# Optimization experiments

Hardware: AMD Instinct MI355X
Metric: run time of the kernel (lower is better)

Reference implementation:

```python
import jax, jax.numpy as jnp
import numpy as np

B, IN_CAPS, IN_DIM = 64, 512, 128
NUM_CAPS, DIM_CAPS, NUM_ROUTING = 32, 32, 3


def squash(x, axis=-1):
    sn = jnp.sum(x * x, axis=axis, keepdims=True)
    return (sn / (1.0 + sn)) * x / (jnp.sqrt(sn) + 1e-8)


def setup_inputs() -> dict:
    key = jax.random.key(0)
    k1, k2, k3 = jax.random.split(key, 3)
    input_tensor = jax.random.normal(k1, (B, IN_CAPS, IN_DIM), dtype=jnp.float32)
    W = 0.001 * jax.random.normal(k2, (NUM_CAPS, IN_DIM, DIM_CAPS), dtype=jnp.float32)
    b0 = jax.random.uniform(k3, (B, NUM_CAPS, IN_CAPS, 1), dtype=jnp.float32)
    return {"input_tensor": input_tensor, "W": W, "b0": b0}


def reference(input_tensor, W, b0):
    # u_hat: (B, num_caps, in_caps, dim_caps)
    u_hat = jnp.einsum('bid,ndc->bnic', input_tensor, W)
    temp_u_hat = jax.lax.stop_gradient(u_hat)
    b = b0
    for _ in range(NUM_ROUTING - 1):
        c = jax.nn.softmax(b, axis=1)            # (B, num_caps, in_caps, 1)
        s = jnp.sum(c * temp_u_hat, axis=2)      # (B, num_caps, dim_caps)
        v = squash(s)
        uv = jnp.einsum('bnic,bnc->bni', temp_u_hat, v)[..., None]
        b = b + uv
    c = jax.nn.softmax(b, axis=1)
    s = jnp.sum(c * u_hat, axis=2)
    return squash(s)                             # (B, num_caps, dim_caps)
```

## Files before the change

### kernel.cpp

```cpp
#include <hip/hip_runtime.h>
#include <math.h>

#define Bsz 64
#define IC  512
#define KD  128
#define NC  32
#define DC  32
#define CHUNK 64
#define NCH   8
#define NBLK  512
#define NTHR  256
#define NTHRB 128

#define CSTR 36
#define BSTR 68
#define WSTR 33

#define CXP_SZ (Bsz * NCH * NC * KD)
#define WV_SZ  (Bsz * NC * KD)

__device__ __forceinline__ int xaddr(int i, int kq) {
    return i * KD + ((((kq) + (i >> 2)) & 31) << 2);
}

__global__ __launch_bounds__(NTHR)
void kACX(const float* __restrict__ bb_in, const float* __restrict__ x_g,
          const float* __restrict__ wv_g, float* __restrict__ bb_out,
          float* __restrict__ cxp, int do_uv, int write_bb)
{
    __shared__ float x_s[CHUNK * KD];
    __shared__ float bb_s[NC * BSTR];
    __shared__ float scr[KD * CSTR];

    const int t = threadIdx.x, blk = blockIdx.x;
    const int b = blk >> 3, ch = blk & 7, i0g = ch * CHUNK;

    for (int rep = 0; rep < 8; ++rep) {
        int v = t + rep * NTHR;
        int i = v >> 5, kq = v & 31;
        *(float4*)(x_s + xaddr(i, kq)) =
            *(const float4*)(x_g + ((size_t)(b * IC + i0g + i)) * KD + (kq << 2));
    }
    for (int rep = 0; rep < 2; ++rep) {
        int v = t + rep * NTHR;
        int n = v >> 4, i4 = v & 15;
        *(float4*)(bb_s + n * BSTR + (i4 << 2)) =
            *(const float4*)(bb_in + ((size_t)(b * NC + n)) * IC + i0g + (i4 << 2));
    }
    if (do_uv) {
        for (int rep = 0; rep < 4; ++rep) {
            const int n = t & 31;
            const int k4 = (t >> 5) + (rep << 3);
            float4 v4 = *(const float4*)(wv_g + ((size_t)(b * NC) + n) * KD + (k4 << 2));
            scr[(k4 * 4 + 0) * CSTR + n] = v4.x;
            scr[(k4 * 4 + 1) * CSTR + n] = v4.y;
            scr[(k4 * 4 + 2) * CSTR + n] = v4.z;
            scr[(k4 * 4 + 3) * CSTR + n] = v4.w;
        }
    }
    __syncthreads();

    if (do_uv) {
        if (t < 128) {
            const int tn = t & 7, ti = t >> 3;
            const int n0 = tn << 2, i0 = ti << 2;
            float4 a0 = {0,0,0,0}, a1 = {0,0,0,0}, a2 = {0,0,0,0}, a3 = {0,0,0,0};
            for (int kq = 0; kq < 32; ++kq) {
                const float4 xr0 = *(const float4*)(x_s + xaddr(i0 + 0, kq));
                const float4 xr1 = *(const float4*)(x_s + xaddr(i0 + 1, kq));
                const float4 xr2 = *(const float4*)(x_s + xaddr(i0 + 2, kq));
                const float4 xr3 = *(const float4*)(x_s + xaddr(i0 + 3, kq));
                const float4 w0 = *(const float4*)(scr + (kq * 4 + 0) * CSTR + n0);
                const float4 w1 = *(const float4*)(scr + (kq * 4 + 1) * CSTR + n0);
                const float4 w2 = *(const float4*)(scr + (kq * 4 + 2) * CSTR + n0);
                const float4 w3 = *(const float4*)(scr + (kq * 4 + 3) * CSTR + n0);
                a0.x += xr0.x*w0.x + xr0.y*w1.x + xr0.z*w2.x + xr0.w*w3.x;
                a0.y += xr0.x*w0.y + xr0.y*w1.y + xr0.z*w2.y + xr0.w*w3.y;
                a0.z += xr0.x*w0.z + xr0.y*w1.z + xr0.z*w2.z + xr0.w*w3.z;
                a0.w += xr0.x*w0.w + xr0.y*w1.w + xr0.z*w2.w + xr0.w*w3.w;
                a1.x += xr1.x*w0.x + xr1.y*w1.x + xr1.z*w2.x + xr1.w*w3.x;
                a1.y += xr1.x*w0.y + xr1.y*w1.y + xr1.z*w2.y + xr1.w*w3.y;
                a1.z += xr1.x*w0.z + xr1.y*w1.z + xr1.z*w2.z + xr1.w*w3.z;
                a1.w += xr1.x*w0.w + xr1.y*w1.w + xr1.z*w2.w + xr1.w*w3.w;
                a2.x += xr2.x*w0.x + xr2.y*w1.x + xr2.z*w2.x + xr2.w*w3.x;
                a2.y += xr2.x*w0.y + xr2.y*w1.y + xr2.z*w2.y + xr2.w*w3.y;
                a2.z += xr2.x*w0.z + xr2.y*w1.z + xr2.z*w2.z + xr2.w*w3.z;
                a2.w += xr2.x*w0.w + xr2.y*w1.w + xr2.z*w2.w + xr2.w*w3.w;
                a3.x += xr3.x*w0.x + xr3.y*w1.x + xr3.z*w2.x + xr3.w*w3.x;
                a3.y += xr3.x*w0.y + xr3.y*w1.y + xr3.z*w2.y + xr3.w*w3.y;
                a3.z += xr3.x*w0.z + xr3.y*w1.z + xr3.z*w2.z + xr3.w*w3.z;
                a3.w += xr3.x*w0.w + xr3.y*w1.w + xr3.z*w2.w + xr3.w*w3.w;
            }
            bb_s[(n0+0)*BSTR + i0+0] += a0.x; bb_s[(n0+1)*BSTR + i0+0] += a0.y;
            bb_s[(n0+2)*BSTR + i0+0] += a0.z; bb_s[(n0+3)*BSTR + i0+0] += a0.w;
            bb_s[(n0+0)*BSTR + i0+1] += a1.x; bb_s[(n0+1)*BSTR + i0+1] += a1.y;
            bb_s[(n0+2)*BSTR + i0+1] += a1.z; bb_s[(n0+3)*BSTR + i0+1] += a1.w;
            bb_s[(n0+0)*BSTR + i0+2] += a2.x; bb_s[(n0+1)*BSTR + i0+2] += a2.y;
            bb_s[(n0+2)*BSTR + i0+2] += a2.z; bb_s[(n0+3)*BSTR + i0+2] += a2.w;
            bb_s[(n0+0)*BSTR + i0+3] += a3.x; bb_s[(n0+1)*BSTR + i0+3] += a3.y;
            bb_s[(n0+2)*BSTR + i0+3] += a3.z; bb_s[(n0+3)*BSTR + i0+3] += a3.w;
        }
        __syncthreads();
        if (write_bb) {
            for (int rep = 0; rep < 2; ++rep) {
                int v = t + rep * NTHR;
                int n = v >> 4, i4 = v & 15;
                *(float4*)(bb_out + ((size_t)(b * NC + n)) * IC + i0g + (i4 << 2)) =
                    *(const float4*)(bb_s + n * BSTR + (i4 << 2));
            }
        }
    }

    if (t < CHUNK) {
        const int ii = t;
        float m = -1e30f;
        #pragma unroll
        for (int n = 0; n < NC; ++n) m = fmaxf(m, bb_s[n * BSTR + ii]);
        float e[NC]; float sum = 0.f;
        #pragma unroll
        for (int n = 0; n < NC; ++n) { float ev = __expf(bb_s[n * BSTR + ii] - m); e[n] = ev; sum += ev; }
        const float inv = 1.f / sum;
        float* crow = scr + ii * CSTR;
        #pragma unroll
        for (int n = 0; n < NC; ++n) crow[n] = e[n] * inv;
    }
    __syncthreads();

    const int tn = t & 7, tk = t >> 3;
    const int n0 = tn << 2;
    float4 acc0 = {0,0,0,0}, acc1 = {0,0,0,0}, acc2 = {0,0,0,0}, acc3 = {0,0,0,0};
    for (int ii = 0; ii < CHUNK; ++ii) {
        const float4 c4 = *(const float4*)(scr + ii * CSTR + n0);
        const float4 x4 = *(const float4*)(x_s + xaddr(ii, tk));
        acc0.x += c4.x*x4.x; acc0.y += c4.x*x4.y; acc0.z += c4.x*x4.z; acc0.w += c4.x*x4.w;
        acc1.x += c4.y*x4.x; acc1.y += c4.y*x4.y; acc1.z += c4.y*x4.z; acc1.w += c4.y*x4.w;
        acc2.x += c4.z*x4.x; acc2.y += c4.z*x4.y; acc2.z += c4.z*x4.z; acc2.w += c4.z*x4.w;
        acc3.x += c4.w*x4.x; acc3.y += c4.w*x4.y; acc3.z += c4.w*x4.z; acc3.w += c4.w*x4.w;
    }
    float* base = cxp + ((size_t)(b * NCH + ch)) * NC * KD + (tk << 2);
    *(float4*)(base + (size_t)(n0 + 0) * KD) = acc0;
    *(float4*)(base + (size_t)(n0 + 1) * KD) = acc1;
    *(float4*)(base + (size_t)(n0 + 2) * KD) = acc2;
    *(float4*)(base + (size_t)(n0 + 3) * KD) = acc3;
}

__global__ __launch_bounds__(NTHRB)
void kB(const float* __restrict__ cxp, const float* __restrict__ W_g,
        float* __restrict__ wv_g, float* __restrict__ out_g, int final_)
{
    __shared__ float w_s[KD * WSTR];
    __shared__ float cxs[4 * KD];
    __shared__ float vs_s[4][DC];

    const int t = threadIdx.x, blk = blockIdx.x;
    const int pb_n = blk & 31, pb_b0 = (blk >> 5) * 4;

    for (int rep = 0; rep < 8; ++rep) {
        int v = t + rep * NTHRB;
        int k = v >> 3, d0 = (v & 7) << 2;
        float4 w4 = *(const float4*)(W_g + (size_t)pb_n * KD * DC + (v << 2));
        float* dst = w_s + k * WSTR + d0;
        dst[0] = w4.x; dst[1] = w4.y; dst[2] = w4.z; dst[3] = w4.w;
    }
    {
        const int bsub = t >> 5, k4 = t & 31;
        float4 s4 = {0,0,0,0};
        const float* p = cxp + (((size_t)(pb_b0 + bsub) * NCH) * NC + pb_n) * KD + (k4 << 2);
        #pragma unroll
        for (int c2 = 0; c2 < NCH; ++c2) {
            float4 v4 = *(const float4*)(p + (size_t)c2 * NC * KD);
            s4.x += v4.x; s4.y += v4.y; s4.z += v4.z; s4.w += v4.w;
        }
        *(float4*)(cxs + bsub * KD + (k4 << 2)) = s4;
    }
    __syncthreads();

    const int bsub = t >> 5, d = t & 31;
    float s = 0.f;
    const float* crow = cxs + bsub * KD;
    for (int k = 0; k < KD; ++k) s += crow[k] * w_s[k * WSTR + d];
    float sn = s * s;
    #pragma unroll
    for (int off = 1; off < 32; off <<= 1) sn += __shfl_xor(sn, off, 64);
    const float vv = s * (sn / ((1.f + sn) * (sqrtf(sn) + 1e-8f)));

    if (final_) {
        out_g[((size_t)(pb_b0 + bsub) * NC + pb_n) * DC + d] = vv;
    } else {
        vs_s[bsub][d] = vv;
        __syncthreads();
        const int k = t;
        float a0 = 0.f, a1 = 0.f, a2 = 0.f, a3 = 0.f;
        #pragma unroll
        for (int dd = 0; dd < DC; ++dd) {
            const float wk = w_s[k * WSTR + dd];
            a0 += wk * vs_s[0][dd];
            a1 += wk * vs_s[1][dd];
            a2 += wk * vs_s[2][dd];
            a3 += wk * vs_s[3][dd];
        }
        size_t base = (((size_t)pb_b0 * NC) + pb_n) * KD + k;
        wv_g[base                      ] = a0;
        wv_g[base + 1 * (size_t)NC * KD] = a1;
        wv_g[base + 2 * (size_t)NC * KD] = a2;
        wv_g[base + 3 * (size_t)NC * KD] = a3;
    }
}

extern "C" void kernel_launch(void* const* d_in, const int* in_sizes, int n_in,
                              void* d_out, int out_size, void* d_ws, size_t ws_size,
                              hipStream_t stream) {
    const float* x  = (const float*)d_in[0];
    const float* W  = (const float*)d_in[1];
    const float* b0 = (const float*)d_in[2];
    float* out = (float*)d_out;

    float* cxp   = (float*)d_ws;
    float* wv    = cxp + CXP_SZ;
    float* bb_ws = wv + WV_SZ;

    kACX<<<NBLK, NTHR, 0, stream>>>(b0, x, nullptr, nullptr, cxp, 0, 0);
    kB  <<<NBLK, NTHRB, 0, stream>>>(cxp, W, wv, out, 0);
    kACX<<<NBLK, NTHR, 0, stream>>>(b0, x, wv, bb_ws, cxp, 1, 1);
    kB  <<<NBLK, NTHRB, 0, stream>>>(cxp, W, wv, out, 0);
    kACX<<<NBLK, NTHR, 0, stream>>>(bb_ws, x, wv, nullptr, cxp, 1, 0);
    kB  <<<NBLK, NTHRB, 0, stream>>>(cxp, W, wv, out, 1);
}
```

Measured before the change: 126.9 us.

## Fuse six routing kernels into one persistent kernel with grid barriers

Replaces the three alternating pairs of kACX/kB launches with a single persistent kernel of 256 blocks. The blocks synchronise through atomic-counter grid barriers, which are reset by a memset before the launch. Each block handles two input-capsule chunks per phase and eight batches in the reduce/squash phase. The aim is to remove launch gaps and tail effects between the six launches. In exchange it relies on all 256 blocks being co-resident, halves the block count, and adds spin-wait costs plus a memset launch.

Result: slower. 277.0 us (+118.4%).

```diff
diff --git a/kernel.cpp b/kernel.cpp
--- a/kernel.cpp
+++ b/kernel.cpp
@@ -8,9 +8,8 @@
 #define DC  32
 #define CHUNK 64
 #define NCH   8
-#define NBLK  512
+#define GBLK  256
 #define NTHR  256
-#define NTHRB 128
 
 #define CSTR 36
 #define BSTR 68
@@ -18,192 +17,217 @@
 
 #define CXP_SZ (Bsz * NCH * NC * KD)
 #define WV_SZ  (Bsz * NC * KD)
+#define BB_SZ  (Bsz * NC * IC)
 
 __device__ __forceinline__ int xaddr(int i, int kq) {
     return i * KD + ((((kq) + (i >> 2)) & 31) << 2);
 }
 
-__global__ __launch_bounds__(NTHR)
-void kACX(const float* __restrict__ bb_in, const float* __restrict__ x_g,
-          const float* __restrict__ wv_g, float* __restrict__ bb_out,
-          float* __restrict__ cxp, int do_uv, int write_bb)
+__device__ __forceinline__ void gridbar(unsigned* ctr, int slot) {
+    __syncthreads();
+    if (threadIdx.x == 0) {
+        __threadfence();
+        unsigned* c = ctr + slot;
+        __hip_atomic_fetch_add(c, 1u, __ATOMIC_ACQ_REL, __HIP_MEMORY_SCOPE_AGENT);
+        unsigned tries = 0;
+        while (__hip_atomic_load(c, __ATOMIC_ACQUIRE, __HIP_MEMORY_SCOPE_AGENT) < GBLK &&
+               tries < (1u << 20)) {
+            ++tries;
+            __builtin_amdgcn_s_sleep(4);
+        }
+        __threadfence();
+    }
+    __syncthreads();
+}
+
+__global__ __launch_bounds__(NTHR, 1)
+void capsAll(const float* __restrict__ x_g, const float* __restrict__ W_g,
+             const float* __restrict__ b0_g, float* __restrict__ out_g,
+             float* __restrict__ cxp, float* __restrict__ wv_g,
+             float* __restrict__ bb_ws, unsigned* __restrict__ ctr)
 {
     __shared__ float x_s[CHUNK * KD];
     __shared__ float bb_s[NC * BSTR];
     __shared__ float scr[KD * CSTR];
 
     const int t = threadIdx.x, blk = blockIdx.x;
-    const int b = blk >> 3, ch = blk & 7, i0g = ch * CHUNK;
-
-    for (int rep = 0; rep < 8; ++rep) {
-        int v = t + rep * NTHR;
-        int i = v >> 5, kq = v & 31;
-        *(float4*)(x_s + xaddr(i, kq)) =
-            *(const float4*)(x_g + ((size_t)(b * IC + i0g + i)) * KD + (kq << 2));
-    }
-    for (int rep = 0; rep < 2; ++rep) {
-        int v = t + rep * NTHR;
-        int n = v >> 4, i4 = v & 15;
-        *(float4*)(bb_s + n * BSTR + (i4 << 2)) =
-            *(const float4*)(bb_in + ((size_t)(b * NC + n)) * IC + i0g + (i4 << 2));
-    }
-    if (do_uv) {
-        for (int rep = 0; rep < 4; ++rep) {
-            const int n = t & 31;
-            const int k4 = (t >> 5) + (rep << 3);
-            float4 v4 = *(const float4*)(wv_g + ((size_t)(b * NC) + n) * KD + (k4 << 2));
-            scr[(k4 * 4 + 0) * CSTR + n] = v4.x;
-            scr[(k4 * 4 + 1) * CSTR + n] = v4.y;
-            scr[(k4 * 4 + 2) * CSTR + n] = v4.z;
-            scr[(k4 * 4 + 3) * CSTR + n] = v4.w;
-        }
-    }
-    __syncthreads();
-
-    if (do_uv) {
-        if (t < 128) {
-            const int tn = t & 7, ti = t >> 3;
-            const int n0 = tn << 2, i0 = ti << 2;
-            float4 a0 = {0,0,0,0}, a1 = {0,0,0,0}, a2 = {0,0,0,0}, a3 = {0,0,0,0};
-            for (int kq = 0; kq < 32; ++kq) {
-                const float4 xr0 = *(const float4*)(x_s + xaddr(i0 + 0, kq));
-                const float4 xr1 = *(const float4*)(x_s + xaddr(i0 + 1, kq));
-                const float4 xr2 = *(const float4*)(x_s + xaddr(i0 + 2, kq));
-                const float4 xr3 = *(const float4*)(x_s + xaddr(i0 + 3, kq));
-                const float4 w0 = *(const float4*)(scr + (kq * 4 + 0) * CSTR + n0);
-                const float4 w1 = *(const float4*)(scr + (kq * 4 + 1) * CSTR + n0);
-                const float4 w2 = *(const float4*)(scr + (kq * 4 + 2) * CSTR + n0);
-                const float4 w3 = *(const float4*)(scr + (kq * 4 + 3) * CSTR + n0);
-                a0.x += xr0.x*w0.x + xr0.y*w1.x + xr0.z*w2.x + xr0.w*w3.x;
-                a0.y += xr0.x*w0.y + xr0.y*w1.y + xr0.z*w2.y + xr0.w*w3.y;
-                a0.z += xr0.x*w0.z + xr0.y*w1.z + xr0.z*w2.z + xr0.w*w3.z;
-                a0.w += xr0.x*w0.w + xr0.y*w1.w + xr0.z*w2.w + xr0.w*w3.w;
-                a1.x += xr1.x*w0.x + xr1.y*w1.x + xr1.z*w2.x + xr1.w*w3.x;
-                a1.y += xr1.x*w0.y + xr1.y*w1.y + xr1.z*w2.y + xr1.w*w3.y;
-                a1.z += xr1.x*w0.z + xr1.y*w1.z + xr1.z*w2.z + xr1.w*w3.z;
-                a1.w += xr1.x*w0.w + xr1.y*w1.w + xr1.z*w2.w + xr1.w*w3.w;
-                a2.x += xr2.x*w0.x + xr2.y*w1.x + xr2.z*w2.x + xr2.w*w3.x;
-                a2.y += xr2.x*w0.y + xr2.y*w1.y + xr2.z*w2.y + xr2.w*w3.y;
-                a2.z += xr2.x*w0.z + xr2.y*w1.z + xr2.z*w2.z + xr2.w*w3.z;
-                a2.w += xr2.x*w0.w + xr2.y*w1.w + xr2.z*w2.w + xr2.w*w3.w;
-                a3.x += xr3.x*w0.x + xr3.y*w1.x + xr3.z*w2.x + xr3.w*w3.x;
-                a3.y += xr3.x*w0.y + xr3.y*w1.y + xr3.z*w2.y + xr3.w*w3.y;
-                a3.z += xr3.x*w0.z + xr3.y*w1.z + xr3.z*w2.z + xr3.w*w3.z;
-                a3.w += xr3.x*w0.w + xr3.y*w1.w + xr3.z*w2.w + xr3.w*w3.w;
-            }
-            bb_s[(n0+0)*BSTR + i0+0] += a0.x; bb_s[(n0+1)*BSTR + i0+0] += a0.y;
-            bb_s[(n0+2)*BSTR + i0+0] += a0.z; bb_s[(n0+3)*BSTR + i0+0] += a0.w;
-            bb_s[(n0+0)*BSTR + i0+1] += a1.x; bb_s[(n0+1)*BSTR + i0+1] += a1.y;
-            bb_s[(n0+2)*BSTR + i0+1] += a1.z; bb_s[(n0+3)*BSTR + i0+1] += a1.w;
-            bb_s[(n0+0)*BSTR + i0+2] += a2.x; bb_s[(n0+1)*BSTR + i0+2] += a2.y;
-            bb_s[(n0+2)*BSTR + i0+2] += a2.z; bb_s[(n0+3)*BSTR + i0+2] += a2.w;
-            bb_s[(n0+0)*BSTR + i0+3] += a3.x; bb_s[(n0+1)*BSTR + i0+3] += a3.y;
-            bb_s[(n0+2)*BSTR + i0+3] += a3.z; bb_s[(n0+3)*BSTR + i0+3] += a3.w;
-        }
-        __syncthreads();
-        if (write_bb) {
+    const int b = blk >> 2, chpair = blk & 3;
+    const int pb_n = blk & 31, pb_b0 = (blk >> 5) * 8;
+
+    float* cxs  = x_s;
+    float* vs_s = x_s + 1024;
+    float* w_s  = scr;
+
+    int slot = 0;
+    for (int r = 0; r < 3; ++r) {
+        const float* bb_in = (r <= 1) ? b0_g : bb_ws;
+        const int do_uv = (r > 0), write_bb = (r == 1), final_ = (r == 2);
+
+        for (int sub = 0; sub < 2; ++sub) {
+            const int ch = chpair * 2 + sub, i0g = ch * CHUNK;
+            __syncthreads();
+
+            for (int rep = 0; rep < 8; ++rep) {
+                int v = t + rep * NTHR;
+                int i = v >> 5, kq = v & 31;
+                *(float4*)(x_s + xaddr(i, kq)) =
+                    *(const float4*)(x_g + ((size_t)(b * IC + i0g + i)) * KD + (kq << 2));
+            }
             for (int rep = 0; rep < 2; ++rep) {
                 int v = t + rep * NTHR;
                 int n = v >> 4, i4 = v & 15;
-                *(float4*)(bb_out + ((size_t)(b * NC + n)) * IC + i0g + (i4 << 2)) =
-                    *(const float4*)(bb_s + n * BSTR + (i4 << 2));
+                *(float4*)(bb_s + n * BSTR + (i4 << 2)) =
+                    *(const float4*)(bb_in + ((size_t)(b * NC + n)) * IC + i0g + (i4 << 2));
+            }
+            if (do_uv) {
+                for (int rep = 0; rep < 4; ++rep) {
+                    const int n = t & 31;
+                    const int k4 = (t >> 5) + (rep << 3);
+                    float4 v4 = *(const float4*)(wv_g + ((size_t)(b * NC) + n) * KD + (k4 << 2));
+                    scr[(k4 * 4 + 0) * CSTR + n] = v4.x;
+                    scr[(k4 * 4 + 1) * CSTR + n] = v4.y;
+                    scr[(k4 * 4 + 2) * CSTR + n] = v4.z;
+                    scr[(k4 * 4 + 3) * CSTR + n] = v4.w;
+                }
+            }
+            __syncthreads();
+
+            if (do_uv) {
+                if (t < 128) {
+                    const int tn = t & 7, ti = t >> 3;
+                    const int n0 = tn << 2, i0 = ti << 2;
+                    float4 a0 = {0,0,0,0}, a1 = {0,0,0,0}, a2 = {0,0,0,0}, a3 = {0,0,0,0};
+                    for (int kq = 0; kq < 32; ++kq) {
+                        const float4 xr0 = *(const float4*)(x_s + xaddr(i0 + 0, kq));
+                        const float4 xr1 = *(const float4*)(x_s + xaddr(i0 + 1, kq));
+                        const float4 xr2 = *(const float4*)(x_s + xaddr(i0 + 2, kq));
+                        const float4 xr3 = *(const float4*)(x_s + xaddr(i0 + 3, kq));
+                        const float4 w0 = *(const float4*)(scr + (kq * 4 + 0) * CSTR + n0);
+                        const float4 w1 = *(const float4*)(scr + (kq * 4 + 1) * CSTR + n0);
+                        const float4 w2 = *(const float4*)(scr + (kq * 4 + 2) * CSTR + n0);
+                        const float4 w3 = *(const float4*)(scr + (kq * 4 + 3) * CSTR + n0);
+                        a0.x += xr0.x*w0.x + xr0.y*w1.x + xr0.z*w2.x + xr0.w*w3.x;
+                        a0.y += xr0.x*w0.y + xr0.y*w1.y + xr0.z*w2.y + xr0.w*w3.y;
+                        a0.z += xr0.x*w0.z + xr0.y*w1.z + xr0.z*w2.z + xr0.w*w3.z;
+                        a0.w += xr0.x*w0.w + xr0.y*w1.w + xr0.z*w2.w + xr0.w*w3.w;
+                        a1.x += xr1.x*w0.x + xr1.y*w1.x + xr1.z*w2.x + xr1.w*w3.x;
+                        a1.y += xr1.x*w0.y + xr1.y*w1.y + xr1.z*w2.y + xr1.w*w3.y;
+                        a1.z += xr1.x*w0.z + xr1.y*w1.z + xr1.z*w2.z + xr1.w*w3.z;
+                        a1.w += xr1.x*w0.w + xr1.y*w1.w + xr1.z*w2.w + xr1.w*w3.w;
+                        a2.x += xr2.x*w0.x + xr2.y*w1.x + xr2.z*w2.x + xr2.w*w3.x;
+                        a2.y += xr2.x*w0.y + xr2.y*w1.y + xr2.z*w2.y + xr2.w*w3.y;
+                        a2.z += xr2.x*w0.z + xr2.y*w1.z + xr2.z*w2.z + xr2.w*w3.z;
+                        a2.w += xr2.x*w0.w + xr2.y*w1.w + xr2.z*w2.w + xr2.w*w3.w;
+                        a3.x += xr3.x*w0.x + xr3.y*w1.x + xr3.z*w2.x + xr3.w*w3.x;
+                        a3.y += xr3.x*w0.y + xr3.y*w1.y + xr3.z*w2.y + xr3.w*w3.y;
+                        a3.z += xr3.x*w0.z + xr3.y*w1.z + xr3.z*w2.z + xr3.w*w3.z;
+                        a3.w += xr3.x*w0.w + xr3.y*w1.w + xr3.z*w2.w + xr3.w*w3.w;
+                    }
+                    bb_s[(n0+0)*BSTR + i0+0] += a0.x; bb_s[(n0+1)*BSTR + i0+0] += a0.y;
+                    bb_s[(n0+2)*BSTR + i0+0] += a0.z; bb_s[(n0+3)*BSTR + i0+0] += a0.w;
+                    bb_s[(n0+0)*BSTR + i0+1] += a1.x; bb_s[(n0+1)*BSTR + i0+1] += a1.y;
+                    bb_s[(n0+2)*BSTR + i0+1] += a1.z; bb_s[(n0+3)*BSTR + i0+1] += a1.w;
+                    bb_s[(n0+0)*BSTR + i0+2] += a2.x; bb_s[(n0+1)*BSTR + i0+2] += a2.y;
+                    bb_s[(n0+2)*BSTR + i0+2] += a2.z; bb_s[(n0+3)*BSTR + i0+2] += a2.w;
+                    bb_s[(n0+0)*BSTR + i0+3] += a3.x; bb_s[(n0+1)*BSTR + i0+3] += a3.y;
+                    bb_s[(n0+2)*BSTR + i0+3] += a3.z; bb_s[(n0+3)*BSTR + i0+3] += a3.w;
+                }
+                __syncthreads();
+                if (write_bb) {
+                    for (int rep = 0; rep < 2; ++rep) {
+                        int v = t + rep * NTHR;
+                        int n = v >> 4, i4 = v & 15;
+                        *(float4*)(bb_ws + ((size_t)(b * NC + n)) * IC + i0g + (i4 << 2)) =
+                            *(const float4*)(bb_s + n * BSTR + (i4 << 2));
+                    }
+                }
+            }
+
+            if (t < CHUNK) {
+                const int ii = t;
+                float m = -1e30f;
+                #pragma unroll
+                for (int n = 0; n < NC; ++n) m = fmaxf(m, bb_s[n * BSTR + ii]);
+                float e[NC]; float sum = 0.f;
+                #pragma unroll
+                for (int n = 0; n < NC; ++n) { float ev = __expf(bb_s[n * BSTR + ii] - m); e[n] = ev; sum += ev; }
+                const float inv = 1.f / sum;
+                float* crow = scr + ii * CSTR;
+                #pragma unroll
+                for (int n = 0; n < NC; ++n) crow[n] = e[n] * inv;
+            }
+            __syncthreads();
+
+            {
+                const int tn = t & 7, tk = t >> 3;
+                const int n0 = tn << 2;
+                float4 acc0 = {0,0,0,0}, acc1 = {0,0,0,0}, acc2 = {0,0,0,0}, acc3 = {0,0,0,0};
+                for (int ii = 0; ii < CHUNK; ++ii) {
+                    const float4 c4 = *(const float4*)(scr + ii * CSTR + n0);
+                    const float4 x4 = *(const float4*)(x_s + xaddr(ii, tk));
+                    acc0.x += c4.x*x4.x; acc0.y += c4.x*x4.y; acc0.z += c4.x*x4.z; acc0.w += c4.x*x4.w;
+                    acc1.x += c4.y*x4.x; acc1.y += c4.y*x4.y; acc1.z += c4.y*x4.z; acc1.w += c4.y*x4.w;
+                    acc2.x += c4.z*x4.x; acc2.y += c4.z*x4.y; acc2.z += c4.z*x4.z; acc2.w += c4.z*x4.w;
+                    acc3.x += c4.w*x4.x; acc3.y += c4.w*x4.y; acc3.z += c4.w*x4.z; acc3.w += c4.w*x4.w;
+                }
+                float* base = cxp + ((size_t)(b * NCH + ch)) * NC * KD + (tk << 2);
+                *(float4*)(base + (size_t)(n0 + 0) * KD) = acc0;
+                *(float4*)(base + (size_t)(n0 + 1) * KD) = acc1;
+                *(float4*)(base + (size_t)(n0 + 2) * KD) = acc2;
+                *(float4*)(base + (size_t)(n0 + 3) * KD) = acc3;
             }
         }
-    }
-
-    if (t < CHUNK) {
-        const int ii = t;
-        float m = -1e30f;
-        #pragma unroll
-        for (int n = 0; n < NC; ++n) m = fmaxf(m, bb_s[n * BSTR + ii]);
-        float e[NC]; float sum = 0.f;
-        #pragma unroll
-        for (int n = 0; n < NC; ++n) { float ev = __expf(bb_s[n * BSTR + ii] - m); e[n] = ev; sum += ev; }
-        const float inv = 1.f / sum;
-        float* crow = scr + ii * CSTR;
-        #pragma unroll
-        for (int n = 0; n < NC; ++n) crow[n] = e[n] * inv;
-    }
-    __syncthreads();
-
-    const int tn = t & 7, tk = t >> 3;
-    const int n0 = tn << 2;
-    float4 acc0 = {0,0,0,0}, acc1 = {0,0,0,0}, acc2 = {0,0,0,0}, acc3 = {0,0,0,0};
-    for (int ii = 0; ii < CHUNK; ++ii) {
-        const float4 c4 = *(const float4*)(scr + ii * CSTR + n0);
-        const float4 x4 = *(const float4*)(x_s + xaddr(ii, tk));
-        acc0.x += c4.x*x4.x; acc0.y += c4.x*x4.y; acc0.z += c4.x*x4.z; acc0.w += c4.x*x4.w;
-        acc1.x += c4.y*x4.x; acc1.y += c4.y*x4.y; acc1.z += c4.y*x4.z; acc1.w += c4.y*x4.w;
-        acc2.x += c4.z*x4.x; acc2.y += c4.z*x4.y; acc2.z += c4.z*x4.z; acc2.w += c4.z*x4.w;
-        acc3.x += c4.w*x4.x; acc3.y += c4.w*x4.y; acc3.z += c4.w*x4.z; acc3.w += c4.w*x4.w;
-    }
-    float* base = cxp + ((size_t)(b * NCH + ch)) * NC * KD + (tk << 2);
-    *(float4*)(base + (size_t)(n0 + 0) * KD) = acc0;
-    *(float4*)(base + (size_t)(n0 + 1) * KD) = acc1;
-    *(float4*)(base + (size_t)(n0 + 2) * KD) = acc2;
-    *(float4*)(base + (size_t)(n0 + 3) * KD) = acc3;
-}
-
-__global__ __launch_bounds__(NTHRB)
-void kB(const float* __restrict__ cxp, const float* __restrict__ W_g,
-        float* __restrict__ wv_g, float* __restrict__ out_g, int final_)
-{
-    __shared__ float w_s[KD * WSTR];
-    __shared__ float cxs[4 * KD];
-    __shared__ float vs_s[4][DC];
-
-    const int t = threadIdx.x, blk = blockIdx.x;
-    const int pb_n = blk & 31, pb_b0 = (blk >> 5) * 4;
-
-    for (int rep = 0; rep < 8; ++rep) {
-        int v = t + rep * NTHRB;
-        int k = v >> 3, d0 = (v & 7) << 2;
-        float4 w4 = *(const float4*)(W_g + (size_t)pb_n * KD * DC + (v << 2));
-        float* dst = w_s + k * WSTR + d0;
-        dst[0] = w4.x; dst[1] = w4.y; dst[2] = w4.z; dst[3] = w4.w;
-    }
-    {
-        const int bsub = t >> 5, k4 = t & 31;
-        float4 s4 = {0,0,0,0};
-        const float* p = cxp + (((size_t)(pb_b0 + bsub) * NCH) * NC + pb_n) * KD + (k4 << 2);
-        #pragma unroll
-        for (int c2 = 0; c2 < NCH; ++c2) {
-            float4 v4 = *(const float4*)(p + (size_t)c2 * NC * KD);
-            s4.x += v4.x; s4.y += v4.y; s4.z += v4.z; s4.w += v4.w;
+
+        gridbar(ctr, slot++);
+
+        {
+            for (int rep = 0; rep < 4; ++rep) {
+                int v = t + rep * NTHR;
+                int k = v >> 3, d0 = (v & 7) << 2;
+                float4 w4 = *(const float4*)(W_g + (size_t)pb_n * KD * DC + (v << 2));
+                float* dst = w_s + k * WSTR + d0;
+                dst[0] = w4.x; dst[1] = w4.y; dst[2] = w4.z; dst[3] = w4.w;
+            }
+            {
+                const int bsub = t >> 5, k4 = t & 31;
+                float4 s4 = {0,0,0,0};
+                const float* p = cxp + (((size_t)(pb_b0 + bsub) * NCH) * NC + pb_n) * KD + (k4 << 2);
+                #pragma unroll
+                for (int c2 = 0; c2 < NCH; ++c2) {
+                    float4 v4 = *(const float4*)(p + (size_t)c2 * NC * KD);
+                    s4.x += v4.x; s4.y += v4.y; s4.z += v4.z; s4.w += v4.w;
+                }
+                *(float4*)(cxs + (t >> 5) * KD + (k4 << 2)) = s4;
+            }
+            __syncthreads();
+
+            const int bsub = t >> 5, d = t & 31;
+            float s = 0.f;
+            const float* crow = cxs + bsub * KD;
+            for (int k = 0; k < KD; ++k) s += crow[k] * w_s[k * WSTR + d];
+            float sn = s * s;
+            #pragma unroll
+            for (int off = 1; off < 32; off <<= 1) sn += __shfl_xor(sn, off, 64);
+            const float vv = s * (sn / ((1.f + sn) * (sqrtf(sn) + 1e-8f)));
+
+            if (final_) {
+                out_g[((size_t)(pb_b0 + bsub) * NC + pb_n) * DC + d] = vv;
+            } else {
+                vs_s[bsub * DC + d] = vv;
+                __syncthreads();
+                const int k = t & 127, bg = t >> 7;
+                #pragma unroll
+                for (int q = 0; q < 4; ++q) {
+                    const int bs = bg * 4 + q;
+                    float a = 0.f;
+                    #pragma unroll
+                    for (int dd = 0; dd < DC; ++dd) a += w_s[k * WSTR + dd] * vs_s[bs * DC + dd];
+                    wv_g[((size_t)(pb_b0 + bs) * NC + pb_n) * KD + k] = a;
+                }
+            }
         }
-        *(float4*)(cxs + bsub * KD + (k4 << 2)) = s4;
-    }
-    __syncthreads();
-
-    const int bsub = t >> 5, d = t & 31;
-    float s = 0.f;
-    const float* crow = cxs + bsub * KD;
-    for (int k = 0; k < KD; ++k) s += crow[k] * w_s[k * WSTR + d];
-    float sn = s * s;
-    #pragma unroll
-    for (int off = 1; off < 32; off <<= 1) sn += __shfl_xor(sn, off, 64);
-    const float vv = s * (sn / ((1.f + sn) * (sqrtf(sn) + 1e-8f)));
-
-    if (final_) {
-        out_g[((size_t)(pb_b0 + bsub) * NC + pb_n) * DC + d] = vv;
-    } else {
-        vs_s[bsub][d] = vv;
-        __syncthreads();
-        const int k = t;
-        float a0 = 0.f, a1 = 0.f, a2 = 0.f, a3 = 0.f;
-        #pragma unroll
-        for (int dd = 0; dd < DC; ++dd) {
-            const float wk = w_s[k * WSTR + dd];
-            a0 += wk * vs_s[0][dd];
-            a1 += wk * vs_s[1][dd];
-            a2 += wk * vs_s[2][dd];
-            a3 += wk * vs_s[3][dd];
-        }
-        size_t base = (((size_t)pb_b0 * NC) + pb_n) * KD + k;
-        wv_g[base                      ] = a0;
-        wv_g[base + 1 * (size_t)NC * KD] = a1;
-        wv_g[base + 2 * (size_t)NC * KD] = a2;
-        wv_g[base + 3 * (size_t)NC * KD] = a3;
+
+        if (!final_) gridbar(ctr, slot++);
     }
 }
 
@@ -218,11 +242,8 @@
     float* cxp   = (float*)d_ws;
     float* wv    = cxp + CXP_SZ;
     float* bb_ws = wv + WV_SZ;
-
-    kACX<<<NBLK, NTHR, 0, stream>>>(b0, x, nullptr, nullptr, cxp, 0, 0);
-    kB  <<<NBLK, NTHRB, 0, stream>>>(cxp, W, wv, out, 0);
-    kACX<<<NBLK, NTHR, 0, stream>>>(b0, x, wv, bb_ws, cxp, 1, 1);
-    kB  <<<NBLK, NTHRB, 0, stream>>>(cxp, W, wv, out, 0);
-    kACX<<<NBLK, NTHR, 0, stream>>>(bb_ws, x, wv, nullptr, cxp, 1, 0);
-    kB  <<<NBLK, NTHRB, 0, stream>>>(cxp, W, wv, out, 1);
-}
+    unsigned* ctr = (unsigned*)(bb_ws + BB_SZ);
+
+    hipMemsetAsync(ctr, 0, 8 * sizeof(unsigned), stream);
+    capsAll<<<GBLK, NTHR, 0, stream>>>(x, W, b0, out, cxp, wv, bb_ws, ctr);
+}
```
